# Kernel optimization log

Measured on AMD Instinct MI355X. Metric: run time of the kernel, lower is better.

## Reference

```python
import jax, jax.numpy as jnp
import numpy as np

# FP4 (e2m1) representable magnitudes: {0, 0.5, 1, 1.5, 2, 3, 4, 6}
_FP4_GRID = np.array([0.0, 0.5, 1.0, 1.5, 2.0, 3.0, 4.0, 6.0], dtype=np.float32)
_FP4_MIDS = (_FP4_GRID[1:] + _FP4_GRID[:-1]) / 2.0  # decision boundaries


def quant_fp4(x):
    """Per-tensor symmetric quantize-dequantize to FP4 e2m1 grid."""
    grid = jnp.asarray(_FP4_GRID, dtype=x.dtype)
    mids = jnp.asarray(_FP4_MIDS, dtype=x.dtype)
    scale = jnp.maximum(jnp.max(jnp.abs(x)) / 6.0, jnp.asarray(1e-12, x.dtype))
    xs = jnp.abs(x) / scale
    idx = jnp.searchsorted(mids, xs)  # nearest-grid-point index
    return jnp.sign(x) * grid[idx] * scale


def fp4_linear(x, w, b):
    # fake-quantized matmul: dequant(FP4(x)) @ dequant(FP4(w)) + b
    return jnp.matmul(quant_fp4(x), quant_fp4(w)) + b


def setup_inputs() -> dict:
    key = jax.random.key(0)
    k1, k2, k3 = jax.random.split(key, 3)
    B, D_IN, D_H, D_OUT = 4096, 4096, 16384, 4096
    x = jax.random.normal(k1, (B, D_IN), dtype=jnp.float32)
    w1 = jax.random.normal(k2, (D_IN, D_H), dtype=jnp.float32)
    b1 = jnp.zeros((D_H,), dtype=jnp.float32)
    w2 = jax.random.normal(k3, (D_H, D_OUT), dtype=jnp.float32)
    b2 = jnp.zeros((D_OUT,), dtype=jnp.float32)
    return {"x": x, "w1": w1, "b1": b1, "w2": w2, "b2": b2}


def reference(x, w1, b1, w2, b2):
    h = jax.nn.relu(fp4_linear(x, w1, b1))
    return fp4_linear(h, w2, b2)
```

## Files before the change

### kernel.cpp

```cpp
#include <hip/hip_runtime.h>
#include <hip/hip_bf16.h>


typedef float f32x4  __attribute__((ext_vector_type(4)));
typedef int   i32x4  __attribute__((ext_vector_type(4)));
typedef int   i32x8  __attribute__((ext_vector_type(8)));

#define AS1 __attribute__((address_space(1)))
#define AS3 __attribute__((address_space(3)))

__device__ __forceinline__ float scale_from_amax_bits(unsigned bits) {
    return fmaxf(__uint_as_float(bits) / 6.0f, 1e-12f);
}

__device__ __forceinline__ unsigned q4(float v, float inv_scale) {
    float xs = fabsf(v) * inv_scale;
    unsigned idx = 0;
    idx += (xs > 0.25f);
    idx += (xs > 0.75f);
    idx += (xs > 1.25f);
    idx += (xs > 1.75f);
    idx += (xs > 2.5f);
    idx += (xs > 3.5f);
    idx += (xs > 5.0f);
    return idx | ((v < 0.0f) ? 8u : 0u);
}

__global__ void zero4_kernel(unsigned* p) {
    if (threadIdx.x < 4) p[threadIdx.x] = 0u;
}

__global__ void sentinel_kernel(float* out, long long n) {
    long long i = (long long)blockIdx.x * blockDim.x + threadIdx.x;
    long long stride = (long long)gridDim.x * blockDim.x;
    for (; i < n; i += stride) out[i] = 1e30f;
}

__global__ void absmax_kernel(const float* __restrict__ in, long long n,
                              unsigned* __restrict__ out) {
    long long i = ((long long)blockIdx.x * blockDim.x + threadIdx.x) * 4;
    long long stride = (long long)gridDim.x * blockDim.x * 4;
    float m = 0.0f;
    for (; i < n; i += stride) {
        f32x4 v = *(const f32x4*)&in[i];
        m = fmaxf(m, fmaxf(fmaxf(fabsf(v.x), fabsf(v.y)),
                           fmaxf(fabsf(v.z), fabsf(v.w))));
    }
    #pragma unroll
    for (int off = 32; off > 0; off >>= 1)
        m = fmaxf(m, __shfl_xor(m, off));
    __shared__ float smax[4];
    int lane = threadIdx.x & 63, w = threadIdx.x >> 6;
    if (lane == 0) smax[w] = m;
    __syncthreads();
    if (threadIdx.x == 0) {
        m = fmaxf(fmaxf(smax[0], smax[1]), fmaxf(smax[2], smax[3]));
        atomicMax(out, __float_as_uint(m));
    }
}

__global__ void quant_pack_rev_kernel(const float* __restrict__ in, long long n,
                                      const unsigned* __restrict__ amax,
                                      unsigned* __restrict__ out) {
    float inv = 1.0f / scale_from_amax_bits(*amax);
    long long nw = n >> 3;
    long long gid = (long long)blockIdx.x * blockDim.x + threadIdx.x;
    long long gs = (long long)gridDim.x * blockDim.x;
    for (long long j = nw - 1 - gid; j >= 0; j -= gs) {
        long long i = j * 8;
        f32x4 a = __builtin_nontemporal_load((const f32x4*)&in[i]);
        f32x4 b = __builtin_nontemporal_load((const f32x4*)&in[i + 4]);
        unsigned u = q4(a.x, inv)        | (q4(a.y, inv) << 4)
                   | (q4(a.z, inv) << 8) | (q4(a.w, inv) << 12)
                   | (q4(b.x, inv) << 16)| (q4(b.y, inv) << 20)
                   | (q4(b.z, inv) << 24)| (q4(b.w, inv) << 28);
        out[j] = u;
    }
}

__global__ void quant_transpose_pack_kernel(const float* __restrict__ in, int R, int C,
                                            const unsigned* __restrict__ amax,
                                            unsigned char* __restrict__ out) {
    __shared__ float tile[64][65];
    float inv = 1.0f / scale_from_amax_bits(*amax);
    int t = threadIdx.x;
    int bid = gridDim.x - 1 - blockIdx.x;
    int CT = C >> 6;
    int tc = bid % CT;
    int tr = bid / CT;
    int r0 = t >> 4;
    int c0 = (t & 15) * 4;
    #pragma unroll
    for (int it = 0; it < 4; ++it) {
        int r = r0 + it * 16;
        f32x4 v = __builtin_nontemporal_load(
            (const f32x4*)&in[(size_t)(tr * 64 + r) * C + tc * 64 + c0]);
        tile[r][c0 + 0] = v.x;
        tile[r][c0 + 1] = v.y;
        tile[r][c0 + 2] = v.z;
        tile[r][c0 + 3] = v.w;
    }
    __syncthreads();
    int c = t >> 2;
    int rch = (t & 3) * 16;
    unsigned u0 = 0, u1 = 0;
    #pragma unroll
    for (int j = 0; j < 8; ++j) u0 |= q4(tile[rch + j][c], inv) << (4 * j);
    #pragma unroll
    for (int j = 0; j < 8; ++j) u1 |= q4(tile[rch + 8 + j][c], inv) << (4 * j);
    uint2 o; o.x = u0; o.y = u1;
    *(uint2*)&out[(size_t)(tc * 64 + c) * (R >> 1) + (size_t)(tr * 32) + (rch >> 1)] = o;
}

__device__ __forceinline__ f32x4 mm16(i32x4 a, i32x4 b, f32x4 c) {
    i32x8 a8 = {a[0], a[1], a[2], a[3], 0, 0, 0, 0};
    i32x8 b8 = {b[0], b[1], b[2], b[3], 0, 0, 0, 0};
    return __builtin_amdgcn_mfma_scale_f32_16x16x128_f8f6f4(
        a8, b8, c, 4, 4, 0, 0x7f7f7f7f, 0, 0x7f7f7f7f);
}

#define AMAX_EPILOG                                                           \
    if (FUSE_AMAX) {                                                          \
        _Pragma("unroll")                                                     \
        for (int off = 32; off > 0; off >>= 1)                                \
            vmax = fmaxf(vmax, __shfl_xor(vmax, off));                        \
        if (lane == 0) smax[wid] = vmax;                                      \
        __syncthreads();                                                      \
        if (tid == 0) {                                                       \
            vmax = fmaxf(fmaxf(smax[0], smax[1]), fmaxf(smax[2], smax[3]));   \
            atomicMax(amaxOut, __float_as_uint(vmax));                        \
        }                                                                     \
    }

template <int RELU, int FUSE_AMAX>
__global__ __launch_bounds__(256, 2)
void gemm_fp4_g1(const unsigned char* __restrict__ Ap,
                 const unsigned char* __restrict__ Bp,
                 float* __restrict__ C, const float* __restrict__ bias,
                 const unsigned* __restrict__ amaxA,
                 const unsigned* __restrict__ amaxB,
                 unsigned* __restrict__ amaxOut,
                 int M, int N, int K) {
    __shared__ alignas(16) unsigned char As[128 * 128];
    __shared__ alignas(16) unsigned char Bs[128 * 128];
    __shared__ float smax[4];

    int nwg = gridDim.x, cpx = nwg >> 3;
    int wg = (blockIdx.x & 7) * cpx + (blockIdx.x >> 3);
    int MT = M >> 7;
    int tm = wg % MT, tn = wg / MT;

    int tid = threadIdx.x, lane = tid & 63, wid = tid >> 6;
    int wr = wid >> 1, wc = wid & 1;

    size_t Kb = (size_t)(K >> 1);

    int cs = ((lane & 7) ^ ((lane >> 3) & 7)) << 4;
    int srow = wid * 32 + (lane >> 3);
    const unsigned char* Abase = Ap + (size_t)(tm * 128 + srow) * Kb + cs;
    const unsigned char* Bbase = Bp + (size_t)(tn * 128 + srow) * Kb + cs;
    char* AsB = (char*)As;
    char* BsB = (char*)Bs;
    int ldsOff = wid * 4096;

    f32x4 acc[4][4] = {};
    int rrA = wr * 64 + (lane & 15);
    int rrB = wc * 64 + (lane & 15);

    int KT = K >> 8;
    for (int kt = 0; kt < KT; ++kt) {
        #pragma unroll
        for (int i = 0; i < 4; ++i) {
            __builtin_amdgcn_global_load_lds(
                (const AS1 void*)(Abase + (size_t)kt * 128 + (size_t)(i * 8) * Kb),
                (AS3 void*)(AsB + ldsOff + i * 1024), 16, 0, 0);
            __builtin_amdgcn_global_load_lds(
                (const AS1 void*)(Bbase + (size_t)kt * 128 + (size_t)(i * 8) * Kb),
                (AS3 void*)(BsB + ldsOff + i * 1024), 16, 0, 0);
        }
        __syncthreads();

        #pragma unroll
        for (int ks = 0; ks < 2; ++ks) {
            int slotOff = ((ks * 4 + (lane >> 4)) ^ (lane & 7)) << 4;
            i32x4 a[4], b[4];
            #pragma unroll
            for (int mi = 0; mi < 4; ++mi)
                a[mi] = *(const i32x4*)(AsB + (rrA + mi * 16) * 128 + slotOff);
            #pragma unroll
            for (int ni = 0; ni < 4; ++ni)
                b[ni] = *(const i32x4*)(BsB + (rrB + ni * 16) * 128 + slotOff);
            #pragma unroll
            for (int mi = 0; mi < 4; ++mi)
                #pragma unroll
                for (int ni = 0; ni < 4; ++ni)
                    acc[mi][ni] = mm16(a[mi], b[ni], acc[mi][ni]);
        }
        __syncthreads();
    }

    float s = scale_from_amax_bits(*amaxA) * scale_from_amax_bits(*amaxB);
    float vmax = 0.0f;
    int rowBase = tm * 128 + wr * 64 + (lane >> 4) * 4;
    int colBase = tn * 128 + wc * 64 + (lane & 15);
    #pragma unroll
    for (int mi = 0; mi < 4; ++mi) {
        #pragma unroll
        for (int ni = 0; ni < 4; ++ni) {
            int col = colBase + ni * 16;
            float bv = bias[col];
            int row = rowBase + mi * 16;
            #pragma unroll
            for (int r = 0; r < 4; ++r) {
                float v = acc[mi][ni][r] * s + bv;
                if (RELU) v = fmaxf(v, 0.0f);
                if (FUSE_AMAX) vmax = fmaxf(vmax, fabsf(v));
                __builtin_nontemporal_store(v, &C[(size_t)(row + r) * N + col]);
            }
        }
    }
    AMAX_EPILOG
}

template <int RELU, int FUSE_AMAX>
__global__ __launch_bounds__(256, 2)
void gemm_fp4_g2(const unsigned char* __restrict__ Ap,
                 const unsigned char* __restrict__ Bp,
                 float* __restrict__ C, const float* __restrict__ bias,
                 const unsigned* __restrict__ amaxA,
                 const unsigned* __restrict__ amaxB,
                 unsigned* __restrict__ amaxOut,
                 int M, int N, int K) {
    __shared__ alignas(16) unsigned char As[2][128 * 64];
    __shared__ alignas(16) unsigned char Bs[2][128 * 64];
    __shared__ float smax[4];

    int nwg = gridDim.x, cpx = nwg >> 3;
    int wg = (blockIdx.x & 7) * cpx + (blockIdx.x >> 3);
    int MT = M >> 7;
    int tm = wg % MT, tn = wg / MT;

    int tid = threadIdx.x, lane = tid & 63, wid = tid >> 6;
    int wr = wid >> 1, wc = wid & 1;

    size_t Kb = (size_t)(K >> 1);

    int csw = ((tid & 3) ^ ((tid >> 3) & 3)) << 4;
    int srow = tid >> 2;
    const unsigned char* Abase = Ap + (size_t)(tm * 128 + srow) * Kb + csw;
    const unsigned char* Bbase = Bp + (size_t)(tn * 128 + srow) * Kb + csw;
    char* AsB = (char*)As;
    char* BsB = (char*)Bs;
    int dstOff = wid << 10;

#define STAGE_G2(d, kt)                                                       \
    do {                                                                      \
        _Pragma("unroll")                                                     \
        for (int i_ = 0; i_ < 2; ++i_) {                                      \
            __builtin_amdgcn_global_load_lds(                                 \
                (const AS1 void*)(Abase + (size_t)(kt) * 64 +                 \
                                  (size_t)(i_ * 64) * Kb),                    \
                (AS3 void*)(AsB + ((d) << 13) + (i_ << 12) + dstOff),         \
                16, 0, 0);                                                    \
            __builtin_amdgcn_global_load_lds(                                 \
                (const AS1 void*)(Bbase + (size_t)(kt) * 64 +                 \
                                  (size_t)(i_ * 64) * Kb),                    \
                (AS3 void*)(BsB + ((d) << 13) + (i_ << 12) + dstOff),         \
                16, 0, 0);                                                    \
        }                                                                     \
    } while (0)

    f32x4 acc[4][4] = {};
    int rrA = wr * 64 + (lane & 15);
    int rrB = wc * 64 + (lane & 15);
    int slotOff = (((lane >> 4) ^ ((lane >> 1) & 3)) << 4);

    int KT = K >> 7;
    STAGE_G2(0, 0);
    __syncthreads();

    for (int t = 0; t < KT; ++t) {
        int d = t & 1;
        if (t + 1 < KT) STAGE_G2(d ^ 1, t + 1);
        __builtin_amdgcn_sched_barrier(0);

        const char* Aq = AsB + (d << 13);
        const char* Bq = BsB + (d << 13);
        i32x4 a[4], b[4];
        #pragma unroll
        for (int mi = 0; mi < 4; ++mi)
            a[mi] = *(const i32x4*)(Aq + (rrA + mi * 16) * 64 + slotOff);
        #pragma unroll
        for (int ni = 0; ni < 4; ++ni)
            b[ni] = *(const i32x4*)(Bq + (rrB + ni * 16) * 64 + slotOff);
        #pragma unroll
        for (int mi = 0; mi < 4; ++mi)
            #pragma unroll
            for (int ni = 0; ni < 4; ++ni)
                acc[mi][ni] = mm16(a[mi], b[ni], acc[mi][ni]);
        __syncthreads();
    }
#undef STAGE_G2

    float s = scale_from_amax_bits(*amaxA) * scale_from_amax_bits(*amaxB);
    float vmax = 0.0f;
    int rowBase = tm * 128 + wr * 64 + (lane >> 4) * 4;
    int colBase = tn * 128 + wc * 64 + (lane & 15);
    #pragma unroll
    for (int mi = 0; mi < 4; ++mi) {
        #pragma unroll
        for (int ni = 0; ni < 4; ++ni) {
            int col = colBase + ni * 16;
            float bv = bias[col];
            int row = rowBase + mi * 16;
            #pragma unroll
            for (int r = 0; r < 4; ++r) {
                float v = acc[mi][ni][r] * s + bv;
                if (RELU) v = fmaxf(v, 0.0f);
                if (FUSE_AMAX) vmax = fmaxf(vmax, fabsf(v));
                __builtin_nontemporal_store(v, &C[(size_t)(row + r) * N + col]);
            }
        }
    }
    AMAX_EPILOG
}

extern "C" void kernel_launch(void* const* d_in, const int* in_sizes, int n_in,
                              void* d_out, int out_size, void* d_ws, size_t ws_size,
                              hipStream_t stream) {
    const float* x  = (const float*)d_in[0];
    const float* w1 = (const float*)d_in[1];
    const float* b1 = (const float*)d_in[2];
    const float* w2 = (const float*)d_in[3];
    const float* b2 = (const float*)d_in[4];
    float* out = (float*)d_out;

    const int B = 4096, DIN = 4096, DH = 16384, DOUT = 4096;

    const size_t off_amax = 0;
    const size_t off_Xq   = 256;
    const size_t off_W    = off_Xq + (size_t)B * DIN / 2;
    const size_t off_h    = off_W + (size_t)DIN * DH / 2;
    const size_t off_Hq   = off_h + (size_t)B * DH * 4;
    const size_t needed   = off_Hq + (size_t)B * DH / 2;

    if (ws_size < needed) {
        sentinel_kernel<<<2048, 256, 0, stream>>>(out, (long long)out_size);
        return;
    }

    char* ws = (char*)d_ws;
    unsigned* amax = (unsigned*)(ws + off_amax);
    unsigned char* Xq = (unsigned char*)(ws + off_Xq);
    unsigned char* Wq = (unsigned char*)(ws + off_W);
    float*         h  = (float*)(ws + off_h);
    unsigned char* Hq = (unsigned char*)(ws + off_Hq);

    zero4_kernel<<<1, 64, 0, stream>>>(amax);

    absmax_kernel<<<2048, 256, 0, stream>>>(w1, (long long)DIN * DH, amax + 1);
    quant_transpose_pack_kernel<<<(DIN / 64) * (DH / 64), 256, 0, stream>>>(
        w1, DIN, DH, amax + 1, Wq);

    absmax_kernel<<<2048, 256, 0, stream>>>(x, (long long)B * DIN, amax + 0);
    quant_pack_rev_kernel<<<2048, 256, 0, stream>>>(x, (long long)B * DIN,
                                                    amax + 0, (unsigned*)Xq);

    gemm_fp4_g1<1, 1><<<(B / 128) * (DH / 128), 256, 0, stream>>>(
        Xq, Wq, h, b1, amax + 0, amax + 1, amax + 2, B, DH, DIN);

    quant_pack_rev_kernel<<<2048, 256, 0, stream>>>(h, (long long)B * DH,
                                                    amax + 2, (unsigned*)Hq);

    absmax_kernel<<<2048, 256, 0, stream>>>(w2, (long long)DH * DOUT, amax + 3);
    quant_transpose_pack_kernel<<<(DH / 64) * (DOUT / 64), 256, 0, stream>>>(
        w2, DH, DOUT, amax + 3, Wq);

    gemm_fp4_g2<0, 0><<<(B / 128) * (DOUT / 128), 256, 0, stream>>>(
        Hq, Wq, out, b2, amax + 2, amax + 3, nullptr, B, DOUT, DH);
}
```

Before: 670.0 us.

## Rewrite second FP4 GEMM with 256x256 tiles, 8 waves, ping-pong pipelined schedule

Replaces the second GEMM kernel with a 512-thread, 256x256-tile version that prefetches two K-steps ahead and splits each step into four MFMA phases. Those phases are interleaved with LDS reads and global-to-LDS loads using explicit barriers, waitcnts and setprio. The goal is more data reuse per tile and better overlap of memory traffic with matrix-core work. In exchange it uses more LDS and registers per block and launches only 256 workgroups, which may leave some compute units underfilled.

```diff
diff --git a/kernel.cpp b/kernel.cpp
--- a/kernel.cpp
+++ b/kernel.cpp
@@ -8,6 +8,10 @@
 
 #define AS1 __attribute__((address_space(1)))
 #define AS3 __attribute__((address_space(3)))
+
+#define SB0   __builtin_amdgcn_sched_barrier(0)
+#define BAR   __builtin_amdgcn_s_barrier()
+#define LGKM0 asm volatile("s_waitcnt lgkmcnt(0)" ::: "memory")
 
 __device__ __forceinline__ float scale_from_amax_bits(unsigned bits) {
     return fmaxf(__uint_as_float(bits) / 6.0f, 1e-12f);
@@ -119,19 +123,6 @@
         a8, b8, c, 4, 4, 0, 0x7f7f7f7f, 0, 0x7f7f7f7f);
 }
 
-#define AMAX_EPILOG                                                           \
-    if (FUSE_AMAX) {                                                          \
-        _Pragma("unroll")                                                     \
-        for (int off = 32; off > 0; off >>= 1)                                \
-            vmax = fmaxf(vmax, __shfl_xor(vmax, off));                        \
-        if (lane == 0) smax[wid] = vmax;                                      \
-        __syncthreads();                                                      \
-        if (tid == 0) {                                                       \
-            vmax = fmaxf(fmaxf(smax[0], smax[1]), fmaxf(smax[2], smax[3]));   \
-            atomicMax(amaxOut, __float_as_uint(vmax));                        \
-        }                                                                     \
-    }
-
 template <int RELU, int FUSE_AMAX>
 __global__ __launch_bounds__(256, 2)
 void gemm_fp4_g1(const unsigned char* __restrict__ Ap,
@@ -219,95 +210,141 @@
             }
         }
     }
-    AMAX_EPILOG
-}
-
-template <int RELU, int FUSE_AMAX>
-__global__ __launch_bounds__(256, 2)
-void gemm_fp4_g2(const unsigned char* __restrict__ Ap,
-                 const unsigned char* __restrict__ Bp,
-                 float* __restrict__ C, const float* __restrict__ bias,
-                 const unsigned* __restrict__ amaxA,
-                 const unsigned* __restrict__ amaxB,
-                 unsigned* __restrict__ amaxOut,
-                 int M, int N, int K) {
-    __shared__ alignas(16) unsigned char As[2][128 * 64];
-    __shared__ alignas(16) unsigned char Bs[2][128 * 64];
-    __shared__ float smax[4];
+    if (FUSE_AMAX) {
+        #pragma unroll
+        for (int off = 32; off > 0; off >>= 1)
+            vmax = fmaxf(vmax, __shfl_xor(vmax, off));
+        if (lane == 0) smax[wid] = vmax;
+        __syncthreads();
+        if (tid == 0) {
+            vmax = fmaxf(fmaxf(smax[0], smax[1]), fmaxf(smax[2], smax[3]));
+            atomicMax(amaxOut, __float_as_uint(vmax));
+        }
+    }
+}
+
+__global__ __launch_bounds__(512, 2)
+void gemm_fp4_g2p(const unsigned char* __restrict__ Ap,
+                  const unsigned char* __restrict__ Bp,
+                  float* __restrict__ C, const float* __restrict__ bias,
+                  const unsigned* __restrict__ amaxA,
+                  const unsigned* __restrict__ amaxB,
+                  int M, int N, int K) {
+    __shared__ alignas(16) unsigned char As[2][256 * 64];
+    __shared__ alignas(16) unsigned char Bs[2][256 * 64];
 
     int nwg = gridDim.x, cpx = nwg >> 3;
     int wg = (blockIdx.x & 7) * cpx + (blockIdx.x >> 3);
-    int MT = M >> 7;
+    int MT = M >> 8;
     int tm = wg % MT, tn = wg / MT;
 
     int tid = threadIdx.x, lane = tid & 63, wid = tid >> 6;
-    int wr = wid >> 1, wc = wid & 1;
+    int wr = wid >> 2;
+    int wc = wid & 3;
 
     size_t Kb = (size_t)(K >> 1);
 
     int csw = ((tid & 3) ^ ((tid >> 3) & 3)) << 4;
     int srow = tid >> 2;
-    const unsigned char* Abase = Ap + (size_t)(tm * 128 + srow) * Kb + csw;
-    const unsigned char* Bbase = Bp + (size_t)(tn * 128 + srow) * Kb + csw;
+    const unsigned char* Abase = Ap + (size_t)(tm * 256 + srow) * Kb + csw;
+    const unsigned char* Bbase = Bp + (size_t)(tn * 256 + srow) * Kb + csw;
     char* AsB = (char*)As;
     char* BsB = (char*)Bs;
     int dstOff = wid << 10;
 
-#define STAGE_G2(d, kt)                                                       \
-    do {                                                                      \
-        _Pragma("unroll")                                                     \
-        for (int i_ = 0; i_ < 2; ++i_) {                                      \
-            __builtin_amdgcn_global_load_lds(                                 \
-                (const AS1 void*)(Abase + (size_t)(kt) * 64 +                 \
-                                  (size_t)(i_ * 64) * Kb),                    \
-                (AS3 void*)(AsB + ((d) << 13) + (i_ << 12) + dstOff),         \
-                16, 0, 0);                                                    \
-            __builtin_amdgcn_global_load_lds(                                 \
-                (const AS1 void*)(Bbase + (size_t)(kt) * 64 +                 \
-                                  (size_t)(i_ * 64) * Kb),                    \
-                (AS3 void*)(BsB + ((d) << 13) + (i_ << 12) + dstOff),         \
-                16, 0, 0);                                                    \
-        }                                                                     \
-    } while (0)
-
-    f32x4 acc[4][4] = {};
-    int rrA = wr * 64 + (lane & 15);
-    int rrB = wc * 64 + (lane & 15);
+#define STG_A2(d, kt, h)                                                      \
+    __builtin_amdgcn_global_load_lds(                                         \
+        (const AS1 void*)(Abase + (size_t)(kt) * 64 + (size_t)((h) * 128) * Kb), \
+        (AS3 void*)(AsB + ((d) << 14) + ((h) << 13) + dstOff), 16, 0, 0)
+#define STG_B2(d, kt, h)                                                      \
+    __builtin_amdgcn_global_load_lds(                                         \
+        (const AS1 void*)(Bbase + (size_t)(kt) * 64 + (size_t)((h) * 128) * Kb), \
+        (AS3 void*)(BsB + ((d) << 14) + ((h) << 13) + dstOff), 16, 0, 0)
+
+    f32x4 acc[8][4] = {};
+    int l15 = lane & 15;
+    int rrA = wr * 128 + l15;
+    int rrB = wc * 64 + l15;
     int slotOff = (((lane >> 4) ^ ((lane >> 1) & 3)) << 4);
 
     int KT = K >> 7;
-    STAGE_G2(0, 0);
-    __syncthreads();
+
+    STG_A2(0, 0, 0); STG_A2(0, 0, 1); STG_B2(0, 0, 0); STG_B2(0, 0, 1);
+    STG_A2(1, 1, 0); STG_A2(1, 1, 1); STG_B2(1, 1, 0); STG_B2(1, 1, 1);
+    asm volatile("s_waitcnt vmcnt(4)" ::: "memory");
+    BAR;
 
     for (int t = 0; t < KT; ++t) {
         int d = t & 1;
-        if (t + 1 < KT) STAGE_G2(d ^ 1, t + 1);
-        __builtin_amdgcn_sched_barrier(0);
-
-        const char* Aq = AsB + (d << 13);
-        const char* Bq = BsB + (d << 13);
-        i32x4 a[4], b[4];
-        #pragma unroll
-        for (int mi = 0; mi < 4; ++mi)
-            a[mi] = *(const i32x4*)(Aq + (rrA + mi * 16) * 64 + slotOff);
+        const char* Aq = AsB + (d << 14);
+        const char* Bq = BsB + (d << 14);
+        bool pf = (t + 2 < KT);
+        i32x4 a0[4], a1[4], b[4];
+
+        #pragma unroll
+        for (int mi = 0; mi < 4; ++mi)
+            a0[mi] = *(const i32x4*)(Aq + (rrA + mi * 16) * 64 + slotOff);
         #pragma unroll
         for (int ni = 0; ni < 4; ++ni)
             b[ni] = *(const i32x4*)(Bq + (rrB + ni * 16) * 64 + slotOff);
-        #pragma unroll
-        for (int mi = 0; mi < 4; ++mi)
-            #pragma unroll
-            for (int ni = 0; ni < 4; ++ni)
-                acc[mi][ni] = mm16(a[mi], b[ni], acc[mi][ni]);
-        __syncthreads();
-    }
-#undef STAGE_G2
+        SB0; BAR;
+        LGKM0; SB0;
+        __builtin_amdgcn_s_setprio(1);
+        #pragma unroll
+        for (int mi = 0; mi < 4; ++mi)
+            #pragma unroll
+            for (int ni = 0; ni < 2; ++ni)
+                acc[mi][ni] = mm16(a0[mi], b[ni], acc[mi][ni]);
+        __builtin_amdgcn_s_setprio(0);
+        SB0; BAR;
+
+        #pragma unroll
+        for (int mi = 0; mi < 4; ++mi)
+            a1[mi] = *(const i32x4*)(Aq + (rrA + (4 + mi) * 16) * 64 + slotOff);
+        if (pf) { STG_B2(d, t + 2, 0); STG_B2(d, t + 2, 1); }
+        SB0; BAR;
+        __builtin_amdgcn_s_setprio(1);
+        #pragma unroll
+        for (int mi = 0; mi < 4; ++mi)
+            #pragma unroll
+            for (int ni = 2; ni < 4; ++ni)
+                acc[mi][ni] = mm16(a0[mi], b[ni], acc[mi][ni]);
+        __builtin_amdgcn_s_setprio(0);
+        SB0;
+        LGKM0;
+        BAR;
+
+        if (pf) { STG_A2(d, t + 2, 0); STG_A2(d, t + 2, 1); }
+        SB0; BAR;
+        __builtin_amdgcn_s_setprio(1);
+        #pragma unroll
+        for (int mi = 0; mi < 4; ++mi)
+            #pragma unroll
+            for (int ni = 0; ni < 2; ++ni)
+                acc[4 + mi][ni] = mm16(a1[mi], b[ni], acc[4 + mi][ni]);
+        __builtin_amdgcn_s_setprio(0);
+        SB0; BAR;
+
+        __builtin_amdgcn_s_setprio(1);
+        #pragma unroll
+        for (int mi = 0; mi < 4; ++mi)
+            #pragma unroll
+            for (int ni = 2; ni < 4; ++ni)
+                acc[4 + mi][ni] = mm16(a1[mi], b[ni], acc[4 + mi][ni]);
+        __builtin_amdgcn_s_setprio(0);
+        SB0;
+        if (pf) { asm volatile("s_waitcnt vmcnt(4)" ::: "memory"); }
+        else    { asm volatile("s_waitcnt vmcnt(0)" ::: "memory"); }
+        BAR;
+    }
+#undef STG_A2
+#undef STG_B2
 
     float s = scale_from_amax_bits(*amaxA) * scale_from_amax_bits(*amaxB);
-    float vmax = 0.0f;
-    int rowBase = tm * 128 + wr * 64 + (lane >> 4) * 4;
-    int colBase = tn * 128 + wc * 64 + (lane & 15);
-    #pragma unroll
-    for (int mi = 0; mi < 4; ++mi) {
+    int rowBase = tm * 256 + wr * 128 + (lane >> 4) * 4;
+    int colBase = tn * 256 + wc * 64 + l15;
+    #pragma unroll
+    for (int mi = 0; mi < 8; ++mi) {
         #pragma unroll
         for (int ni = 0; ni < 4; ++ni) {
             int col = colBase + ni * 16;
@@ -316,13 +353,10 @@
             #pragma unroll
             for (int r = 0; r < 4; ++r) {
                 float v = acc[mi][ni][r] * s + bv;
-                if (RELU) v = fmaxf(v, 0.0f);
-                if (FUSE_AMAX) vmax = fmaxf(vmax, fabsf(v));
                 __builtin_nontemporal_store(v, &C[(size_t)(row + r) * N + col]);
             }
         }
     }
-    AMAX_EPILOG
 }
 
 extern "C" void kernel_launch(void* const* d_in, const int* in_sizes, int n_in,
@@ -376,6 +410,6 @@
     quant_transpose_pack_kernel<<<(DH / 64) * (DOUT / 64), 256, 0, stream>>>(
         w2, DH, DOUT, amax + 3, Wq);
 
-    gemm_fp4_g2<0, 0><<<(B / 128) * (DOUT / 128), 256, 0, stream>>>(
-        Hq, Wq, out, b2, amax + 2, amax + 3, nullptr, B, DOUT, DH);
-}
+    gemm_fp4_g2p<<<(B / 256) * (DOUT / 256), 512, 0, stream>>>(
+        Hq, Wq, out, b2, amax + 2, amax + 3, B, DOUT, DH);
+}
```

After: 663.6 us. About the same (-1.0%).
